# Optimization experiments

Measured on AMD Instinct MI355X. Metric: run time of the kernel, lower is better.

## Reference

```python
import jax, jax.numpy as jnp
import numpy as np

N = 100000
E = 800000
IN_FEATS = 128
H_FEATS = 128
HEADS = 4
OUT = H_FEATS // HEADS  # 32
NEG_SLOPE = 0.2  # DGL GATConv default


def gat_conv(x, src, dst, W, attn_l, attn_r, bias):
    """DGL-style GATConv. x: [N, F_in] -> [N, HEADS, OUT]."""
    h = (x @ W).reshape(N, HEADS, OUT)                      # projected features
    el = jnp.sum(h * attn_l, axis=-1)                       # [N, H]
    er = jnp.sum(h * attn_r, axis=-1)                       # [N, H]
    e = jax.nn.leaky_relu(el[src] + er[dst], NEG_SLOPE)     # [E, H] edge logits
    # edge softmax over incoming edges of each dst node
    m = jax.ops.segment_max(e, dst, num_segments=N)          # [N, H]
    ex = jnp.exp(e - m[dst])                                 # [E, H]
    s = jax.ops.segment_sum(ex, dst, num_segments=N)         # [N, H]
    a = ex / s[dst]                                          # [E, H]
    msg = h[src] * a[:, :, None]                             # [E, H, OUT]
    out = jax.ops.segment_sum(msg, dst, num_segments=N)      # [N, H, OUT]
    return out + bias.reshape(1, HEADS, OUT)


def setup_inputs() -> dict:
    key = jax.random.key(0)
    ks = jax.random.split(key, 12)
    feat = jax.random.normal(ks[0], (N, IN_FEATS), dtype=jnp.float32)
    src = jax.random.randint(ks[1], (E,), 0, N)
    dst = jax.random.randint(ks[2], (E,), 0, N)
    s1 = 1.0 / np.sqrt(IN_FEATS)
    s2 = 1.0 / np.sqrt(H_FEATS)
    return {
        "feat": feat,
        "src": src,
        "dst": dst,
        "W1": jax.random.normal(ks[3], (IN_FEATS, HEADS * OUT), dtype=jnp.float32) * s1,
        "al1": jax.random.normal(ks[4], (HEADS, OUT), dtype=jnp.float32) * s2,
        "ar1": jax.random.normal(ks[5], (HEADS, OUT), dtype=jnp.float32) * s2,
        "b1": jnp.zeros((HEADS * OUT,), dtype=jnp.float32),
        "W2": jax.random.normal(ks[6], (H_FEATS, HEADS * OUT), dtype=jnp.float32) * s2,
        "al2": jax.random.normal(ks[7], (HEADS, OUT), dtype=jnp.float32) * s2,
        "ar2": jax.random.normal(ks[8], (HEADS, OUT), dtype=jnp.float32) * s2,
        "b2": jnp.zeros((HEADS * OUT,), dtype=jnp.float32),
    }


def reference(feat, src, dst, W1, al1, ar1, b1, W2, al2, ar2, b2):
    h = gat_conv(feat, src, dst, W1, al1, ar1, b1).reshape(N, H_FEATS)  # flatten(1)
    h = jax.nn.relu(h)
    h = gat_conv(h, src, dst, W2, al2, ar2, b2).mean(axis=1)            # mean over heads
    return h
```

## Files before the change

### kernel.cpp

```cpp
#include <hip/hip_runtime.h>
#include <math.h>

#define N_NODES 100000
#define N_EDGES 800000
#define NEG_SLOPE 0.2f
#define GEMM_BLOCKS 782
#define HIST_BLOCKS 3125

typedef __attribute__((ext_vector_type(8))) short short8;
typedef __attribute__((ext_vector_type(4))) float floatx4;

__device__ __forceinline__ float lrelu(float x) { return x > 0.f ? x : NEG_SLOPE * x; }

__device__ __forceinline__ unsigned bf16_rne(float f) {
    unsigned u = __float_as_uint(f);
    return (u + 0x7fffu + ((u >> 16) & 1u)) >> 16;
}
__device__ __forceinline__ unsigned bfpack(float lo, float hi) {
    return bf16_rne(lo) | (bf16_rne(hi) << 16);
}
__device__ __forceinline__ float bflo(unsigned p) { return __uint_as_float(p << 16); }
__device__ __forceinline__ float bfhi(unsigned p) { return __uint_as_float(p & 0xffff0000u); }

__global__ __launch_bounds__(256) void k_prep0(const float* __restrict__ W1,
                                               const float* __restrict__ al1,
                                               const float* __restrict__ ar1,
                                               const float* __restrict__ W2,
                                               const float* __restrict__ al2,
                                               const float* __restrict__ ar2,
                                               unsigned short* __restrict__ wt1,
                                               unsigned short* __restrict__ wt2,
                                               unsigned short* __restrict__ et1,
                                               unsigned short* __restrict__ et2,
                                               int* __restrict__ deg,
                                               int* __restrict__ done) {
    int b = blockIdx.x, tid = threadIdx.x;
    if (b < 128) {
        int t2 = b * 256 + tid;
        const float* W = (t2 < 16384) ? W1 : W2;
        unsigned short* wt = (t2 < 16384) ? wt1 : wt2;
        int t = t2 & 16383;
        int n = t >> 7, k = t & 127;
        wt[t] = (unsigned short)bf16_rne(W[k * 128 + n]);
    } else if (b < 130) {
        const float* W = (b == 128) ? W1 : W2;
        const float* al = (b == 128) ? al1 : al2;
        const float* ar = (b == 128) ? ar1 : ar2;
        unsigned short* et = (b == 128) ? et1 : et2;
        for (int o = tid * 8; o < tid * 8 + 8; o++) {
            int n = o >> 7, k = o & 127;
            float sacc = 0.f;
            if (n < 8) {
                const float* a = (n < 4) ? al : ar;
                int hh = n & 3;
                #pragma unroll 8
                for (int c = 0; c < 32; c++)
                    sacc += W[k * 128 + hh * 32 + c] * a[hh * 32 + c];
            }
            et[n * 128 + k] = (unsigned short)bf16_rne(sacc);
        }
    } else if (b < 228) {
        int i = (b - 130) * 1024 + tid * 4;
        if (i + 3 < N_NODES) *(int4*)&deg[i] = make_int4(0, 0, 0, 0);
        else { for (int j = i; j < N_NODES; j++) if (j >= 0) deg[j] = 0; }
    } else {
        if (tid < 64) done[tid] = 0;
    }
}

__device__ __forceinline__ void gemm_tile(int base, const void* __restrict__ Xv,
                                          const unsigned short* __restrict__ wt,
                                          const unsigned short* __restrict__ et,
                                          unsigned* __restrict__ Hb,
                                          float* __restrict__ EL,
                                          float* __restrict__ ER,
                                          int src_bf16,
                                          unsigned short* wsh,
                                          unsigned short* esh) {
    int tid = threadIdx.x;
    int w = tid >> 6, lane = tid & 63;
    int q = lane >> 4, nl = lane & 15;

    const uint4* wt4 = (const uint4*)wt;
    #pragma unroll
    for (int i = 0; i < 8; i++) {
        int idx = tid + i * 256;
        int rn = idx >> 4, c8 = idx & 15;
        int kc = c8 >> 2, qq = c8 & 3;
        int slot = rn * 128 + ((kc ^ ((rn >> 2) & 3)) * 4 + (qq ^ (rn & 3))) * 8;
        *(uint4*)&wsh[slot] = wt4[idx];
    }
    {
        const uint4* et4 = (const uint4*)et;
        int rn = tid >> 4, c8 = tid & 15;
        *(uint4*)&esh[rn * 136 + c8 * 8] = et4[tid];
    }

    short8 afr[2][4];
    int row0 = base + w * 32 + nl;
    if (!src_bf16) {
        const float4* X4 = (const float4*)Xv;
        #pragma unroll
        for (int rt = 0; rt < 2; rt++) {
            int rr = row0 + rt * 16; if (rr > N_NODES - 1) rr = N_NODES - 1;
            const float4* px = X4 + (size_t)rr * 32 + q * 2;
            #pragma unroll
            for (int kc = 0; kc < 4; kc++) {
                float4 u = px[kc * 8], v = px[kc * 8 + 1];
                short8 f;
                f[0] = (short)bf16_rne(u.x); f[1] = (short)bf16_rne(u.y);
                f[2] = (short)bf16_rne(u.z); f[3] = (short)bf16_rne(u.w);
                f[4] = (short)bf16_rne(v.x); f[5] = (short)bf16_rne(v.y);
                f[6] = (short)bf16_rne(v.z); f[7] = (short)bf16_rne(v.w);
                afr[rt][kc] = f;
            }
        }
    } else {
        const unsigned short* Xb = (const unsigned short*)Xv;
        #pragma unroll
        for (int rt = 0; rt < 2; rt++) {
            int rr = row0 + rt * 16; if (rr > N_NODES - 1) rr = N_NODES - 1;
            #pragma unroll
            for (int kc = 0; kc < 4; kc++)
                afr[rt][kc] = *(const short8*)(Xb + (size_t)rr * 128 + kc * 32 + q * 8);
        }
    }

    floatx4 acc[2][8];
    floatx4 acc_e[2];
    #pragma unroll
    for (int rt = 0; rt < 2; rt++) {
        acc_e[rt] = (floatx4){0.f, 0.f, 0.f, 0.f};
        #pragma unroll
        for (int ct = 0; ct < 8; ct++)
            acc[rt][ct] = (floatx4){0.f, 0.f, 0.f, 0.f};
    }

    __syncthreads();

    int sw_hi = (nl >> 2) & 3, sw_lo = nl & 3;
    #pragma unroll
    for (int ct = 0; ct < 8; ct++) {
        int rbase = (ct * 16 + nl) * 128;
        #pragma unroll
        for (int kc = 0; kc < 4; kc++) {
            short8 b = *(const short8*)&wsh[rbase + ((kc ^ sw_hi) * 4 + (q ^ sw_lo)) * 8];
            acc[0][ct] = __builtin_amdgcn_mfma_f32_16x16x32_bf16(afr[0][kc], b, acc[0][ct], 0, 0, 0);
            acc[1][ct] = __builtin_amdgcn_mfma_f32_16x16x32_bf16(afr[1][kc], b, acc[1][ct], 0, 0, 0);
        }
    }
    #pragma unroll
    for (int kc = 0; kc < 4; kc++) {
        short8 e8 = *(const short8*)&esh[nl * 136 + (kc * 4 + q) * 8];
        acc_e[0] = __builtin_amdgcn_mfma_f32_16x16x32_bf16(afr[0][kc], e8, acc_e[0], 0, 0, 0);
        acc_e[1] = __builtin_amdgcn_mfma_f32_16x16x32_bf16(afr[1][kc], e8, acc_e[1], 0, 0, 0);
    }

    #pragma unroll
    for (int rt = 0; rt < 2; rt++) {
        #pragma unroll
        for (int r = 0; r < 4; r++) {
            int row = base + w * 32 + rt * 16 + q * 4 + r;
            bool valid = row < N_NODES;
            unsigned* hrow = Hb + (size_t)row * 64;
            #pragma unroll
            for (int ct = 0; ct < 8; ct++) {
                float vlo = acc[rt][ct][r];
                float vhi = __shfl_down(vlo, 1);
                if (valid && !(nl & 1)) hrow[ct * 8 + (nl >> 1)] = bfpack(vlo, vhi);
            }
            if (valid && nl < 8) {
                float v = acc_e[rt][r];
                if (nl < 4) EL[row * 4 + nl] = v;
                else        ER[row * 4 + (nl & 3)] = v;
            }
        }
    }
}

__global__ __launch_bounds__(256) void k_gemm_hist(const float* __restrict__ feat,
                                                   const unsigned short* __restrict__ wt1,
                                                   const unsigned short* __restrict__ et1,
                                                   unsigned* __restrict__ Hb,
                                                   float* __restrict__ EL,
                                                   float* __restrict__ ER,
                                                   const int* __restrict__ dst,
                                                   int* __restrict__ deg) {
    __shared__ unsigned short wsh[128 * 128];
    __shared__ unsigned short esh[16 * 136];
    int b = blockIdx.x;
    if (b < GEMM_BLOCKS) {
        gemm_tile(b * 128, feat, wt1, et1, Hb, EL, ER, 0, wsh, esh);
    } else {
        int e = (b - GEMM_BLOCKS) * 256 + threadIdx.x;
        if (e < N_EDGES) atomicAdd(&deg[dst[e]], 1);
    }
}

__global__ __launch_bounds__(256) void k_gemm(const void* __restrict__ Xv,
                                              const unsigned short* __restrict__ wt,
                                              const unsigned short* __restrict__ et,
                                              unsigned* __restrict__ Hb,
                                              float* __restrict__ EL,
                                              float* __restrict__ ER,
                                              int src_bf16) {
    __shared__ unsigned short wsh[128 * 128];
    __shared__ unsigned short esh[16 * 136];
    gemm_tile(blockIdx.x * 128, Xv, wt, et, Hb, EL, ER, src_bf16, wsh, esh);
}

__global__ __launch_bounds__(256) void k_scan(const int* __restrict__ deg,
                                              int* __restrict__ rs,
                                              int* __restrict__ cursor,
                                              int* __restrict__ bsums,
                                              int* __restrict__ done) {
    __shared__ int sd[256];
    int tid = threadIdx.x, b = blockIdx.x;
    int base = b * 1024 + tid * 4;
    int v0 = (base + 0 < N_NODES) ? deg[base + 0] : 0;
    int v1 = (base + 1 < N_NODES) ? deg[base + 1] : 0;
    int v2 = (base + 2 < N_NODES) ? deg[base + 2] : 0;
    int v3 = (base + 3 < N_NODES) ? deg[base + 3] : 0;
    int t = v0 + v1 + v2 + v3;
    sd[tid] = t;
    __syncthreads();
    int incl = t;
    for (int off = 1; off < 256; off <<= 1) {
        int x = (tid >= off) ? sd[tid - off] : 0;
        __syncthreads();
        incl += x;
        sd[tid] = incl;
        __syncthreads();
    }
    int excl = incl - t;

    if (tid == 255) {
        atomicExch(&bsums[b], incl);
        __threadfence();
        atomicAdd(done, 1);
    }
    if (tid == 0) {
        while (atomicAdd(done, 0) < 98) { }
    }
    __syncthreads();

    int bv = (tid < b) ? atomicAdd(&bsums[tid], 0) : 0;
    __syncthreads();
    sd[tid] = bv;
    __syncthreads();
    for (int off = 128; off > 0; off >>= 1) {
        if (tid < off) sd[tid] += sd[tid + off];
        __syncthreads();
    }
    int boff = sd[0];

    int p0 = excl + boff;
    if (base + 0 < N_NODES) { rs[base + 0] = p0; cursor[base + 0] = p0; }
    if (base + 1 < N_NODES) { rs[base + 1] = p0 + v0; cursor[base + 1] = p0 + v0; }
    if (base + 2 < N_NODES) { rs[base + 2] = p0 + v0 + v1; cursor[base + 2] = p0 + v0 + v1; }
    if (base + 3 < N_NODES) { rs[base + 3] = p0 + v0 + v1 + v2; cursor[base + 3] = p0 + v0 + v1 + v2; }
    if (b == 0 && tid == 0) rs[N_NODES] = N_EDGES;
}

__global__ void k_scatter(const int* __restrict__ src, const int* __restrict__ dst,
                          int* __restrict__ cursor, int* __restrict__ csr_src) {
    int e = blockIdx.x * blockDim.x + threadIdx.x;
    if (e < N_EDGES) {
        int d = dst[e];
        int p = atomicAdd(&cursor[d], 1);
        csr_src[p] = src[e];
    }
}

__global__ __launch_bounds__(256) void k_gather(const int* __restrict__ rs,
                                                const int* __restrict__ csr_src,
                                                const float* __restrict__ EL,
                                                const float* __restrict__ ER,
                                                const unsigned* __restrict__ Hb,
                                                const float* __restrict__ bias,
                                                void* __restrict__ out,
                                                int final_layer) {
    int wid = (blockIdx.x * blockDim.x + threadIdx.x) >> 6;
    int lane = threadIdx.x & 63;
    int g = lane >> 4, l16 = lane & 15;
    int h = l16 >> 2;
    int n0 = wid * 4;
    if (n0 >= N_NODES) return;
    int nend = min(n0 + 4, N_NODES);

    float bv[8];
    #pragma unroll
    for (int c = 0; c < 8; c++) bv[c] = bias[l16 * 8 + c];

    for (int n = n0; n < nend; n++) {
        int s = rs[n], e = rs[n + 1];
        float erh = ER[n * 4 + h];
        float acc[8];
        #pragma unroll
        for (int c = 0; c < 8; c++) acc[c] = 0.f;
        float sa = 0.f;

        for (int j = s; j < e; j += 8) {
            int j0 = j + g, j1 = j + 4 + g;
            uint4 p0 = make_uint4(0, 0, 0, 0), p1 = make_uint4(0, 0, 0, 0);
            float w0 = 0.f, w1 = 0.f;
            if (j0 < e) {
                int s0 = csr_src[j0];
                p0 = *(const uint4*)(Hb + (size_t)s0 * 64 + l16 * 4);
                w0 = __expf(lrelu(EL[s0 * 4 + h] + erh));
            }
            if (j1 < e) {
                int s1 = csr_src[j1];
                p1 = *(const uint4*)(Hb + (size_t)s1 * 64 + l16 * 4);
                w1 = __expf(lrelu(EL[s1 * 4 + h] + erh));
            }
            sa += w0 + w1;
            acc[0] = fmaf(bflo(p0.x), w0, acc[0]); acc[1] = fmaf(bfhi(p0.x), w0, acc[1]);
            acc[2] = fmaf(bflo(p0.y), w0, acc[2]); acc[3] = fmaf(bfhi(p0.y), w0, acc[3]);
            acc[4] = fmaf(bflo(p0.z), w0, acc[4]); acc[5] = fmaf(bfhi(p0.z), w0, acc[5]);
            acc[6] = fmaf(bflo(p0.w), w0, acc[6]); acc[7] = fmaf(bfhi(p0.w), w0, acc[7]);
            acc[0] = fmaf(bflo(p1.x), w1, acc[0]); acc[1] = fmaf(bfhi(p1.x), w1, acc[1]);
            acc[2] = fmaf(bflo(p1.y), w1, acc[2]); acc[3] = fmaf(bfhi(p1.y), w1, acc[3]);
            acc[4] = fmaf(bflo(p1.z), w1, acc[4]); acc[5] = fmaf(bfhi(p1.z), w1, acc[5]);
            acc[6] = fmaf(bflo(p1.w), w1, acc[6]); acc[7] = fmaf(bfhi(p1.w), w1, acc[7]);
        }

        #pragma unroll
        for (int c = 0; c < 8; c++) {
            acc[c] += __shfl_xor(acc[c], 16);
            acc[c] += __shfl_xor(acc[c], 32);
        }
        sa += __shfl_xor(sa, 16);
        sa += __shfl_xor(sa, 32);
        float inv = (e > s) ? 1.f / sa : 0.f;

        float r[8];
        #pragma unroll
        for (int c = 0; c < 8; c++) r[c] = acc[c] * inv + bv[c];

        if (!final_layer) {
            if (g == 0) {
                uint4 pk;
                pk.x = bfpack(fmaxf(r[0], 0.f), fmaxf(r[1], 0.f));
                pk.y = bfpack(fmaxf(r[2], 0.f), fmaxf(r[3], 0.f));
                pk.z = bfpack(fmaxf(r[4], 0.f), fmaxf(r[5], 0.f));
                pk.w = bfpack(fmaxf(r[6], 0.f), fmaxf(r[7], 0.f));
                *(uint4*)((unsigned*)out + (size_t)n * 64 + l16 * 4) = pk;
            }
        } else {
            #pragma unroll
            for (int c = 0; c < 8; c++) {
                r[c] += __shfl_xor(r[c], 4);
                r[c] += __shfl_xor(r[c], 8);
            }
            if (g == 0 && l16 < 4) {
                float* po = (float*)out + (size_t)n * 32 + l16 * 8;
                *(float4*)po = make_float4(0.25f * r[0], 0.25f * r[1], 0.25f * r[2], 0.25f * r[3]);
                *(float4*)(po + 4) = make_float4(0.25f * r[4], 0.25f * r[5], 0.25f * r[6], 0.25f * r[7]);
            }
        }
    }
}

extern "C" void kernel_launch(void* const* d_in, const int* in_sizes, int n_in,
                              void* d_out, int out_size, void* d_ws, size_t ws_size,
                              hipStream_t stream) {
    const float* feat = (const float*)d_in[0];
    const int* src = (const int*)d_in[1];
    const int* dst = (const int*)d_in[2];
    const float* W1 = (const float*)d_in[3];
    const float* al1 = (const float*)d_in[4];
    const float* ar1 = (const float*)d_in[5];
    const float* b1 = (const float*)d_in[6];
    const float* W2 = (const float*)d_in[7];
    const float* al2 = (const float*)d_in[8];
    const float* ar2 = (const float*)d_in[9];
    const float* b2 = (const float*)d_in[10];
    float* out = (float*)d_out;

    char* ws = (char*)d_ws;
    size_t off = 0;
    auto alloc = [&](size_t bytes) {
        void* p = ws + off;
        off += (bytes + 255) & ~(size_t)255;
        return p;
    };
    int* deg = (int*)alloc((size_t)N_NODES * 4);
    int* done = (int*)alloc(256);
    int* rs = (int*)alloc(((size_t)N_NODES + 1) * 4);
    int* cursor = (int*)alloc((size_t)N_NODES * 4);
    int* bsums = (int*)alloc(128 * 4);
    int* csr_src = (int*)alloc((size_t)N_EDGES * 4);
    unsigned* Hb = (unsigned*)alloc((size_t)N_NODES * 64 * 4);
    float* el = (float*)alloc((size_t)N_NODES * 4 * 4);
    float* er = (float*)alloc((size_t)N_NODES * 4 * 4);
    unsigned* out1b = (unsigned*)alloc((size_t)N_NODES * 64 * 4);
    unsigned short* wt1 = (unsigned short*)alloc(128 * 128 * 2);
    unsigned short* wt2 = (unsigned short*)alloc(128 * 128 * 2);
    unsigned short* et1 = (unsigned short*)alloc(16 * 128 * 2);
    unsigned short* et2 = (unsigned short*)alloc(16 * 128 * 2);

    int gat_blocks = (N_NODES + 15) / 16;

    k_prep0<<<229, 256, 0, stream>>>(W1, al1, ar1, W2, al2, ar2,
                                     wt1, wt2, et1, et2, deg, done);
    k_gemm_hist<<<GEMM_BLOCKS + HIST_BLOCKS, 256, 0, stream>>>(feat, wt1, et1, Hb, el, er,
                                                               dst, deg);
    k_scan<<<98, 256, 0, stream>>>(deg, rs, cursor, bsums, done);
    k_scatter<<<HIST_BLOCKS, 256, 0, stream>>>(src, dst, cursor, csr_src);
    k_gather<<<gat_blocks, 256, 0, stream>>>(rs, csr_src, el, er, Hb, b1, out1b, 0);
    k_gemm<<<GEMM_BLOCKS, 256, 0, stream>>>(out1b, wt2, et2, Hb, el, er, 1);
    k_gather<<<gat_blocks, 256, 0, stream>>>(rs, csr_src, el, er, Hb, b2, out, 1);
}
```

Measured before the change: 315.9 us.

## Map one 16-lane group per destination node in GAT gather kernel

Each wavefront now processes four destination nodes at once, one per 16-lane group, instead of walking four nodes in sequence with the edges of each split across groups. Each group walks its node's edge list eight edges at a time, loading all eight indices and feature rows before accumulating, which gives more loads in flight. This drops the cross-group shuffle reductions and the serial per-node loop. In exchange, lanes diverge when degrees differ within a wavefront, and each lane holds more registers for the eight-edge buffers.

```diff
diff --git a/kernel.cpp b/kernel.cpp
--- a/kernel.cpp
+++ b/kernel.cpp
@@ -282,82 +282,71 @@
                                                 int final_layer) {
     int wid = (blockIdx.x * blockDim.x + threadIdx.x) >> 6;
     int lane = threadIdx.x & 63;
-    int g = lane >> 4, l16 = lane & 15;
-    int h = l16 >> 2;
-    int n0 = wid * 4;
-    if (n0 >= N_NODES) return;
-    int nend = min(n0 + 4, N_NODES);
+    int l = lane & 15;
+    int h = l >> 2;
+    int n = wid * 4 + (lane >> 4);
+    if (n >= N_NODES) return;
+
+    int s = rs[n], e = rs[n + 1];
+    float erh = ER[n * 4 + h];
 
     float bv[8];
     #pragma unroll
-    for (int c = 0; c < 8; c++) bv[c] = bias[l16 * 8 + c];
-
-    for (int n = n0; n < nend; n++) {
-        int s = rs[n], e = rs[n + 1];
-        float erh = ER[n * 4 + h];
-        float acc[8];
-        #pragma unroll
-        for (int c = 0; c < 8; c++) acc[c] = 0.f;
-        float sa = 0.f;
-
-        for (int j = s; j < e; j += 8) {
-            int j0 = j + g, j1 = j + 4 + g;
-            uint4 p0 = make_uint4(0, 0, 0, 0), p1 = make_uint4(0, 0, 0, 0);
-            float w0 = 0.f, w1 = 0.f;
-            if (j0 < e) {
-                int s0 = csr_src[j0];
-                p0 = *(const uint4*)(Hb + (size_t)s0 * 64 + l16 * 4);
-                w0 = __expf(lrelu(EL[s0 * 4 + h] + erh));
+    for (int c = 0; c < 8; c++) bv[c] = bias[l * 8 + c];
+
+    float acc[8];
+    #pragma unroll
+    for (int c = 0; c < 8; c++) acc[c] = 0.f;
+    float sa = 0.f;
+
+    for (int j = s; j < e; j += 8) {
+        int ii[8];
+        #pragma unroll
+        for (int k = 0; k < 8; k++) ii[k] = (j + k < e) ? csr_src[j + k] : -1;
+        uint4 P[8];
+        float W[8];
+        #pragma unroll
+        for (int k = 0; k < 8; k++) {
+            if (ii[k] >= 0) {
+                P[k] = *(const uint4*)(Hb + (size_t)ii[k] * 64 + l * 4);
+                W[k] = __expf(lrelu(EL[ii[k] * 4 + h] + erh));
+            } else {
+                P[k] = make_uint4(0u, 0u, 0u, 0u);
+                W[k] = 0.f;
             }
-            if (j1 < e) {
-                int s1 = csr_src[j1];
-                p1 = *(const uint4*)(Hb + (size_t)s1 * 64 + l16 * 4);
-                w1 = __expf(lrelu(EL[s1 * 4 + h] + erh));
-            }
-            sa += w0 + w1;
-            acc[0] = fmaf(bflo(p0.x), w0, acc[0]); acc[1] = fmaf(bfhi(p0.x), w0, acc[1]);
-            acc[2] = fmaf(bflo(p0.y), w0, acc[2]); acc[3] = fmaf(bfhi(p0.y), w0, acc[3]);
-            acc[4] = fmaf(bflo(p0.z), w0, acc[4]); acc[5] = fmaf(bfhi(p0.z), w0, acc[5]);
-            acc[6] = fmaf(bflo(p0.w), w0, acc[6]); acc[7] = fmaf(bfhi(p0.w), w0, acc[7]);
-            acc[0] = fmaf(bflo(p1.x), w1, acc[0]); acc[1] = fmaf(bfhi(p1.x), w1, acc[1]);
-            acc[2] = fmaf(bflo(p1.y), w1, acc[2]); acc[3] = fmaf(bfhi(p1.y), w1, acc[3]);
-            acc[4] = fmaf(bflo(p1.z), w1, acc[4]); acc[5] = fmaf(bfhi(p1.z), w1, acc[5]);
-            acc[6] = fmaf(bflo(p1.w), w1, acc[6]); acc[7] = fmaf(bfhi(p1.w), w1, acc[7]);
-        }
-
+        }
+        #pragma unroll
+        for (int k = 0; k < 8; k++) {
+            sa += W[k];
+            acc[0] = fmaf(bflo(P[k].x), W[k], acc[0]); acc[1] = fmaf(bfhi(P[k].x), W[k], acc[1]);
+            acc[2] = fmaf(bflo(P[k].y), W[k], acc[2]); acc[3] = fmaf(bfhi(P[k].y), W[k], acc[3]);
+            acc[4] = fmaf(bflo(P[k].z), W[k], acc[4]); acc[5] = fmaf(bfhi(P[k].z), W[k], acc[5]);
+            acc[6] = fmaf(bflo(P[k].w), W[k], acc[6]); acc[7] = fmaf(bfhi(P[k].w), W[k], acc[7]);
+        }
+    }
+
+    float inv = (e > s) ? 1.f / sa : 0.f;
+    float r[8];
+    #pragma unroll
+    for (int c = 0; c < 8; c++) r[c] = acc[c] * inv + bv[c];
+
+    if (!final_layer) {
+        uint4 pk;
+        pk.x = bfpack(fmaxf(r[0], 0.f), fmaxf(r[1], 0.f));
+        pk.y = bfpack(fmaxf(r[2], 0.f), fmaxf(r[3], 0.f));
+        pk.z = bfpack(fmaxf(r[4], 0.f), fmaxf(r[5], 0.f));
+        pk.w = bfpack(fmaxf(r[6], 0.f), fmaxf(r[7], 0.f));
+        *(uint4*)((unsigned*)out + (size_t)n * 64 + l * 4) = pk;
+    } else {
         #pragma unroll
         for (int c = 0; c < 8; c++) {
-            acc[c] += __shfl_xor(acc[c], 16);
-            acc[c] += __shfl_xor(acc[c], 32);
-        }
-        sa += __shfl_xor(sa, 16);
-        sa += __shfl_xor(sa, 32);
-        float inv = (e > s) ? 1.f / sa : 0.f;
-
-        float r[8];
-        #pragma unroll
-        for (int c = 0; c < 8; c++) r[c] = acc[c] * inv + bv[c];
-
-        if (!final_layer) {
-            if (g == 0) {
-                uint4 pk;
-                pk.x = bfpack(fmaxf(r[0], 0.f), fmaxf(r[1], 0.f));
-                pk.y = bfpack(fmaxf(r[2], 0.f), fmaxf(r[3], 0.f));
-                pk.z = bfpack(fmaxf(r[4], 0.f), fmaxf(r[5], 0.f));
-                pk.w = bfpack(fmaxf(r[6], 0.f), fmaxf(r[7], 0.f));
-                *(uint4*)((unsigned*)out + (size_t)n * 64 + l16 * 4) = pk;
-            }
-        } else {
-            #pragma unroll
-            for (int c = 0; c < 8; c++) {
-                r[c] += __shfl_xor(r[c], 4);
-                r[c] += __shfl_xor(r[c], 8);
-            }
-            if (g == 0 && l16 < 4) {
-                float* po = (float*)out + (size_t)n * 32 + l16 * 8;
-                *(float4*)po = make_float4(0.25f * r[0], 0.25f * r[1], 0.25f * r[2], 0.25f * r[3]);
-                *(float4*)(po + 4) = make_float4(0.25f * r[4], 0.25f * r[5], 0.25f * r[6], 0.25f * r[7]);
-            }
+            r[c] += __shfl_xor(r[c], 4);
+            r[c] += __shfl_xor(r[c], 8);
+        }
+        if (l < 4) {
+            float* po = (float*)out + (size_t)n * 32 + l * 8;
+            *(float4*)po = make_float4(0.25f * r[0], 0.25f * r[1], 0.25f * r[2], 0.25f * r[3]);
+            *(float4*)(po + 4) = make_float4(0.25f * r[4], 0.25f * r[5], 0.25f * r[6], 0.25f * r[7]);
         }
     }
 }
```

New measurement: 329.7 us. 4.4% more time.

## Move histogram into prep kernel and fuse CSR scatter with layer-1 GEMM

Applied to the files above, without the earlier changes.

Zeroing of the degree and done buffers moves to a hipMemsetAsync. The degree histogram now runs inside the weight-prep kernel, and the CSR scatter runs in the same launch as the first-layer GEMM. This drops one kernel launch and lets the atomic-heavy scatter overlap with the compute-bound GEMM blocks. The cost is an extra memset node and a heavier prep kernel, which now sits on the critical path before the scan.

```diff
diff --git a/kernel.cpp b/kernel.cpp
--- a/kernel.cpp
+++ b/kernel.cpp
@@ -22,18 +22,18 @@
 __device__ __forceinline__ float bflo(unsigned p) { return __uint_as_float(p << 16); }
 __device__ __forceinline__ float bfhi(unsigned p) { return __uint_as_float(p & 0xffff0000u); }
 
-__global__ __launch_bounds__(256) void k_prep0(const float* __restrict__ W1,
-                                               const float* __restrict__ al1,
-                                               const float* __restrict__ ar1,
-                                               const float* __restrict__ W2,
-                                               const float* __restrict__ al2,
-                                               const float* __restrict__ ar2,
-                                               unsigned short* __restrict__ wt1,
-                                               unsigned short* __restrict__ wt2,
-                                               unsigned short* __restrict__ et1,
-                                               unsigned short* __restrict__ et2,
-                                               int* __restrict__ deg,
-                                               int* __restrict__ done) {
+__global__ __launch_bounds__(256) void k_prep_hist(const float* __restrict__ W1,
+                                                   const float* __restrict__ al1,
+                                                   const float* __restrict__ ar1,
+                                                   const float* __restrict__ W2,
+                                                   const float* __restrict__ al2,
+                                                   const float* __restrict__ ar2,
+                                                   unsigned short* __restrict__ wt1,
+                                                   unsigned short* __restrict__ wt2,
+                                                   unsigned short* __restrict__ et1,
+                                                   unsigned short* __restrict__ et2,
+                                                   const int* __restrict__ dst,
+                                                   int* __restrict__ deg) {
     int b = blockIdx.x, tid = threadIdx.x;
     if (b < 128) {
         int t2 = b * 256 + tid;
@@ -59,12 +59,9 @@
             }
             et[n * 128 + k] = (unsigned short)bf16_rne(sacc);
         }
-    } else if (b < 228) {
-        int i = (b - 130) * 1024 + tid * 4;
-        if (i + 3 < N_NODES) *(int4*)&deg[i] = make_int4(0, 0, 0, 0);
-        else { for (int j = i; j < N_NODES; j++) if (j >= 0) deg[j] = 0; }
     } else {
-        if (tid < 64) done[tid] = 0;
+        int e = (b - 130) * 256 + tid;
+        if (e < N_EDGES) atomicAdd(&deg[dst[e]], 1);
     }
 }
 
@@ -178,14 +175,16 @@
     }
 }
 
-__global__ __launch_bounds__(256) void k_gemm_hist(const float* __restrict__ feat,
-                                                   const unsigned short* __restrict__ wt1,
-                                                   const unsigned short* __restrict__ et1,
-                                                   unsigned* __restrict__ Hb,
-                                                   float* __restrict__ EL,
-                                                   float* __restrict__ ER,
-                                                   const int* __restrict__ dst,
-                                                   int* __restrict__ deg) {
+__global__ __launch_bounds__(256) void k_gemm_scatter(const float* __restrict__ feat,
+                                                      const unsigned short* __restrict__ wt1,
+                                                      const unsigned short* __restrict__ et1,
+                                                      unsigned* __restrict__ Hb,
+                                                      float* __restrict__ EL,
+                                                      float* __restrict__ ER,
+                                                      const int* __restrict__ src,
+                                                      const int* __restrict__ dst,
+                                                      int* __restrict__ cursor,
+                                                      int* __restrict__ csr_src) {
     __shared__ unsigned short wsh[128 * 128];
     __shared__ unsigned short esh[16 * 136];
     int b = blockIdx.x;
@@ -193,7 +192,11 @@
         gemm_tile(b * 128, feat, wt1, et1, Hb, EL, ER, 0, wsh, esh);
     } else {
         int e = (b - GEMM_BLOCKS) * 256 + threadIdx.x;
-        if (e < N_EDGES) atomicAdd(&deg[dst[e]], 1);
+        if (e < N_EDGES) {
+            int d = dst[e];
+            int p = atomicAdd(&cursor[d], 1);
+            csr_src[p] = src[e];
+        }
     }
 }
 
@@ -262,16 +265,6 @@
     if (b == 0 && tid == 0) rs[N_NODES] = N_EDGES;
 }
 
-__global__ void k_scatter(const int* __restrict__ src, const int* __restrict__ dst,
-                          int* __restrict__ cursor, int* __restrict__ csr_src) {
-    int e = blockIdx.x * blockDim.x + threadIdx.x;
-    if (e < N_EDGES) {
-        int d = dst[e];
-        int p = atomicAdd(&cursor[d], 1);
-        csr_src[p] = src[e];
-    }
-}
-
 __global__ __launch_bounds__(256) void k_gather(const int* __restrict__ rs,
                                                 const int* __restrict__ csr_src,
                                                 const float* __restrict__ EL,
@@ -387,6 +380,7 @@
     };
     int* deg = (int*)alloc((size_t)N_NODES * 4);
     int* done = (int*)alloc(256);
+    size_t zero_bytes = off;
     int* rs = (int*)alloc(((size_t)N_NODES + 1) * 4);
     int* cursor = (int*)alloc((size_t)N_NODES * 4);
     int* bsums = (int*)alloc(128 * 4);
@@ -402,12 +396,12 @@
 
     int gat_blocks = (N_NODES + 15) / 16;
 
-    k_prep0<<<229, 256, 0, stream>>>(W1, al1, ar1, W2, al2, ar2,
-                                     wt1, wt2, et1, et2, deg, done);
-    k_gemm_hist<<<GEMM_BLOCKS + HIST_BLOCKS, 256, 0, stream>>>(feat, wt1, et1, Hb, el, er,
-                                                               dst, deg);
+    hipMemsetAsync(ws, 0, zero_bytes, stream);
+    k_prep_hist<<<130 + HIST_BLOCKS, 256, 0, stream>>>(W1, al1, ar1, W2, al2, ar2,
+                                                       wt1, wt2, et1, et2, dst, deg);
     k_scan<<<98, 256, 0, stream>>>(deg, rs, cursor, bsums, done);
-    k_scatter<<<HIST_BLOCKS, 256, 0, stream>>>(src, dst, cursor, csr_src);
+    k_gemm_scatter<<<GEMM_BLOCKS + HIST_BLOCKS, 256, 0, stream>>>(feat, wt1, et1, Hb, el, er,
+                                                                  src, dst, cursor, csr_src);
     k_gather<<<gat_blocks, 256, 0, stream>>>(rs, csr_src, el, er, Hb, b1, out1b, 0);
     k_gemm<<<GEMM_BLOCKS, 256, 0, stream>>>(out1b, wt2, et2, Hb, el, er, 1);
     k_gather<<<gat_blocks, 256, 0, stream>>>(rs, csr_src, el, er, Hb, b2, out, 1);
```

New measurement: 324.3 us. +2.6%, slower.

## Fuse CSR scan and edge scatter into one kernel with a grid barrier

Applied to the files above, without the earlier changes.

Merges the prefix-scan kernel and the edge-scatter kernel into one launch. A second software grid barrier on done[1] separates the two phases. The scatter then runs as a grid-stride loop over the 98 scan blocks, with four edges per iteration to overlap the atomic latency. This saves one kernel launch and its gap, but the atomic-heavy scatter now runs on far fewer wavefronts than the original 3125 blocks, and it relies on done[1] being zeroed beforehand.

```diff
diff --git a/kernel.cpp b/kernel.cpp
--- a/kernel.cpp
+++ b/kernel.cpp
@@ -6,6 +6,7 @@
 #define NEG_SLOPE 0.2f
 #define GEMM_BLOCKS 782
 #define HIST_BLOCKS 3125
+#define SCAN_BLOCKS 98
 
 typedef __attribute__((ext_vector_type(8))) short short8;
 typedef __attribute__((ext_vector_type(4))) float floatx4;
@@ -209,11 +210,14 @@
     gemm_tile(blockIdx.x * 128, Xv, wt, et, Hb, EL, ER, src_bf16, wsh, esh);
 }
 
-__global__ __launch_bounds__(256) void k_scan(const int* __restrict__ deg,
-                                              int* __restrict__ rs,
-                                              int* __restrict__ cursor,
-                                              int* __restrict__ bsums,
-                                              int* __restrict__ done) {
+__global__ __launch_bounds__(256) void k_scan_scatter(const int* __restrict__ deg,
+                                                      int* __restrict__ rs,
+                                                      int* __restrict__ cursor,
+                                                      int* __restrict__ bsums,
+                                                      int* __restrict__ done,
+                                                      const int* __restrict__ src,
+                                                      const int* __restrict__ dst,
+                                                      int* __restrict__ csr_src) {
     __shared__ int sd[256];
     int tid = threadIdx.x, b = blockIdx.x;
     int base = b * 1024 + tid * 4;
@@ -237,10 +241,10 @@
     if (tid == 255) {
         atomicExch(&bsums[b], incl);
         __threadfence();
-        atomicAdd(done, 1);
+        atomicAdd(&done[0], 1);
     }
     if (tid == 0) {
-        while (atomicAdd(done, 0) < 98) { }
+        while (atomicAdd(&done[0], 0) < SCAN_BLOCKS) { }
     }
     __syncthreads();
 
@@ -255,17 +259,38 @@
     int boff = sd[0];
 
     int p0 = excl + boff;
-    if (base + 0 < N_NODES) { rs[base + 0] = p0; cursor[base + 0] = p0; }
-    if (base + 1 < N_NODES) { rs[base + 1] = p0 + v0; cursor[base + 1] = p0 + v0; }
-    if (base + 2 < N_NODES) { rs[base + 2] = p0 + v0 + v1; cursor[base + 2] = p0 + v0 + v1; }
-    if (base + 3 < N_NODES) { rs[base + 3] = p0 + v0 + v1 + v2; cursor[base + 3] = p0 + v0 + v1 + v2; }
+    if (base + 0 < N_NODES) { rs[base + 0] = p0;                atomicExch(&cursor[base + 0], p0); }
+    if (base + 1 < N_NODES) { rs[base + 1] = p0 + v0;           atomicExch(&cursor[base + 1], p0 + v0); }
+    if (base + 2 < N_NODES) { rs[base + 2] = p0 + v0 + v1;      atomicExch(&cursor[base + 2], p0 + v0 + v1); }
+    if (base + 3 < N_NODES) { rs[base + 3] = p0 + v0 + v1 + v2; atomicExch(&cursor[base + 3], p0 + v0 + v1 + v2); }
     if (b == 0 && tid == 0) rs[N_NODES] = N_EDGES;
-}
-
-__global__ void k_scatter(const int* __restrict__ src, const int* __restrict__ dst,
-                          int* __restrict__ cursor, int* __restrict__ csr_src) {
-    int e = blockIdx.x * blockDim.x + threadIdx.x;
-    if (e < N_EDGES) {
+
+    __threadfence();
+    __syncthreads();
+    if (tid == 0) {
+        atomicAdd(&done[1], 1);
+        while (atomicAdd(&done[1], 0) < SCAN_BLOCKS) { }
+    }
+    __syncthreads();
+
+    const int stride = SCAN_BLOCKS * 256;
+    int e = b * 256 + tid;
+    while (e + 3 * stride < N_EDGES) {
+        int d0 = dst[e];             int s0 = src[e];
+        int d1 = dst[e + stride];    int s1 = src[e + stride];
+        int d2 = dst[e + 2*stride];  int s2 = src[e + 2*stride];
+        int d3 = dst[e + 3*stride];  int s3 = src[e + 3*stride];
+        int q0 = atomicAdd(&cursor[d0], 1);
+        int q1 = atomicAdd(&cursor[d1], 1);
+        int q2 = atomicAdd(&cursor[d2], 1);
+        int q3 = atomicAdd(&cursor[d3], 1);
+        csr_src[q0] = s0;
+        csr_src[q1] = s1;
+        csr_src[q2] = s2;
+        csr_src[q3] = s3;
+        e += 4 * stride;
+    }
+    for (; e < N_EDGES; e += stride) {
         int d = dst[e];
         int p = atomicAdd(&cursor[d], 1);
         csr_src[p] = src[e];
@@ -406,8 +431,8 @@
                                      wt1, wt2, et1, et2, deg, done);
     k_gemm_hist<<<GEMM_BLOCKS + HIST_BLOCKS, 256, 0, stream>>>(feat, wt1, et1, Hb, el, er,
                                                                dst, deg);
-    k_scan<<<98, 256, 0, stream>>>(deg, rs, cursor, bsums, done);
-    k_scatter<<<HIST_BLOCKS, 256, 0, stream>>>(src, dst, cursor, csr_src);
+    k_scan_scatter<<<SCAN_BLOCKS, 256, 0, stream>>>(deg, rs, cursor, bsums, done,
+                                                    src, dst, csr_src);
     k_gather<<<gat_blocks, 256, 0, stream>>>(rs, csr_src, el, er, Hb, b1, out1b, 0);
     k_gemm<<<GEMM_BLOCKS, 256, 0, stream>>>(out1b, wt2, et2, Hb, el, er, 1);
     k_gather<<<gat_blocks, 256, 0, stream>>>(rs, csr_src, el, er, Hb, b2, out, 1);
```

Result: no change. 318.9 us (+0.9%).
